# Optimization experiments

Measured on AMD Instinct MI355X. Metric: run time of the kernel, lower is better.

Reference implementation:

```python
import jax, jax.numpy as jnp
import numpy as np

B, L, H, E = 2, 2048, 16, 64  # S == L (causal self-attention), D == E


def setup_inputs() -> dict:
    key = jax.random.key(0)
    kq, kk, kv, ks = jax.random.split(key, 4)
    queries = jax.random.normal(kq, (B, L, H, E), dtype=jnp.float32)
    keys = jax.random.normal(kk, (B, L, H, E), dtype=jnp.float32)
    values = jax.random.normal(kv, (B, L, H, E), dtype=jnp.float32)
    # TriangularCausalMask: True above the diagonal -> masked out
    attn_mask = jnp.broadcast_to(
        jnp.triu(jnp.ones((L, L), dtype=bool), k=1)[None, None], (B, 1, L, L)
    )
    init_score = jax.random.uniform(ks, (B, L, L), dtype=jnp.float32)
    return {
        "queries": queries,
        "keys": keys,
        "values": values,
        "attn_mask": attn_mask,
        "init_score": init_score,
    }


def reference(queries, keys, values, attn_mask, init_score):
    # queries: [B,L,H,E], keys: [B,S,H,E], values: [B,S,H,D]
    E_ = queries.shape[-1]
    scale = 1.0 / np.sqrt(E_).astype(np.float32)
    # scores: [B,H,L,S]
    scores = jnp.einsum('blhe,bshe->bhls', queries, keys)
    scores = jnp.where(attn_mask, -jnp.inf, scores)
    A = jax.nn.softmax(scale * scores, axis=-1)  # dropout p=0 -> identity
    # post-softmax bias, broadcast over heads
    A = A + 0.1 * init_score[:, None, :, :]
    # V: [B,L,H,D]
    V = jnp.einsum('bhls,bshd->blhd', A, values)
    return V
```

## Files before the change

kernel.cpp:

```cpp
#include <hip/hip_runtime.h>
#include <hip/hip_bf16.h>
#include <math.h>

#define BB 2
#define LL 2048
#define HH 16
#define EE 64
#define LOG2E 1.44269504089f

typedef __attribute__((ext_vector_type(8))) short short8;
typedef __attribute__((ext_vector_type(4))) float floatx4;
typedef unsigned int u32;

union S8 { short8 v; u32 u[4]; ushort4 q[2]; };

__device__ inline u32 pkbf(float lo, float hi) {
    union { __hip_bfloat162 h; u32 u; } c;
    c.h = __float22bfloat162_rn(make_float2(lo, hi));
    return c.u;
}

__device__ inline ushort4 cvt4(float4 v) {
    union { __hip_bfloat162 h; u32 u; } a, b;
    a.h = __float22bfloat162_rn(make_float2(v.x, v.y));
    b.h = __float22bfloat162_rn(make_float2(v.z, v.w));
    ushort4 r;
    r.x = (unsigned short)(a.u & 0xffffu);
    r.y = (unsigned short)(a.u >> 16);
    r.z = (unsigned short)(b.u & 0xffffu);
    r.w = (unsigned short)(b.u >> 16);
    return r;
}

__device__ inline short8 pack8(float4 a, float4 b) {
    S8 s; s.q[0] = cvt4(a); s.q[1] = cvt4(b); return s.v;
}

__device__ inline void async16(unsigned short* lds, const unsigned short* g) {
    __builtin_amdgcn_global_load_lds(
        (const __attribute__((address_space(1))) u32*)g,
        (__attribute__((address_space(3))) u32*)lds, 16, 0, 0);
}

__global__ __launch_bounds__(256) void prepass(
    const float* __restrict__ k, const float* __restrict__ v,
    const float* __restrict__ isc, unsigned short* __restrict__ kb,
    unsigned short* __restrict__ vt, unsigned short* __restrict__ isb)
{
    const int bid = blockIdx.x;
    const int t = threadIdx.x;
    if (bid < 1024) {
        #pragma unroll
        for (int it = 0; it < 4; ++it) {
            int idx = bid * 1024 + it * 256 + t;
            float4 val = ((const float4*)k)[idx];
            int e4 = idx & 15, h = (idx >> 4) & 15, l = (idx >> 8) & 2047, b = idx >> 19;
            *(ushort4*)&kb[(((b * 16 + h) * 2048 + l) * 64) + e4 * 4] = cvt4(val);
        }
    } else if (bid < 2048) {
        const int ib = bid - 1024;
        #pragma unroll
        for (int it = 0; it < 8; ++it) {
            int idx = ib * 2048 + it * 256 + t;
            float4 val = ((const float4*)isc)[idx];
            val.x *= 0.1f; val.y *= 0.1f; val.z *= 0.1f; val.w *= 0.1f;
            ((ushort4*)isb)[idx] = cvt4(val);
        }
    } else {
        __shared__ float Tf[64][68];
        const int vb = bid - 2048;
        const int st = vb & 31, h = (vb >> 5) & 15, b = vb >> 9;
        const int s0 = st * 64;
        #pragma unroll
        for (int i = 0; i < 4; ++i) {
            int r = i * 16 + (t >> 4), c = (t & 15) * 4;
            float4 val = *(const float4*)(v + (((b * LL + s0 + r) * HH + h) * EE) + c);
            *(float4*)&Tf[r][c] = val;
        }
        __syncthreads();
        #pragma unroll
        for (int i = 0; i < 4; ++i) {
            int d = i * 16 + (t >> 4), s4 = (t & 15) * 4;
            float4 val = make_float4(Tf[s4 + 0][d], Tf[s4 + 1][d],
                                     Tf[s4 + 2][d], Tf[s4 + 3][d]);
            *(ushort4*)&vt[((b * 16 + h) * 64 + d) * 2048 + s0 + s4] = cvt4(val);
        }
    }
}

template <int MODE>
__device__ __forceinline__ void tile_step(
    const unsigned short* __restrict__ Ks, const unsigned short* __restrict__ Vs,
    const unsigned short* __restrict__ Is,
    const short8 qf[2], floatx4 o_attn[4], floatx4 o_bias[4], float& lsum,
    int s0, int mbase, int wave, int lq, int ln, int lnl,
    int alo, int ahi, bool hisel)
{
    u32 pk[4][2];
    if (MODE < 2) {
        #pragma unroll
        for (int sb = 0; sb < 4; ++sb) {
            if (MODE == 1 && wave < sb) { pk[sb][0] = 0; pk[sb][1] = 0; continue; }
            short8 kf0 = *(const short8*)&Ks[(sb * 16 + ln) * 64 + ((lq ^ lnl) << 3)];
            short8 kf1 = *(const short8*)&Ks[(sb * 16 + ln) * 64 + (((4 + lq) ^ lnl) << 3)];
            floatx4 sa = {0.f, 0.f, 0.f, 0.f};
            sa = __builtin_amdgcn_mfma_f32_16x16x32_bf16(kf0, qf[0], sa, 0, 0, 0);
            sa = __builtin_amdgcn_mfma_f32_16x16x32_bf16(kf1, qf[1], sa, 0, 0, 0);
            float pv[4];
            #pragma unroll
            for (int r = 0; r < 4; ++r) {
                float t = sa[r];
                if (MODE == 1 && (s0 + sb * 16 + lq * 4 + r) > (mbase + ln)) t = -INFINITY;
                float p = exp2f(t);
                lsum += p;
                pv[r] = p;
            }
            pk[sb][0] = pkbf(pv[0], pv[1]);
            pk[sb][1] = pkbf(pv[2], pv[3]);
        }
    }
    #pragma unroll
    for (int kk = 0; kk < 2; ++kk) {
        short8 vf[4];
        #pragma unroll
        for (int db = 0; db < 4; ++db)
            vf[db] = *(const short8*)&Vs[(db * 16 + ln) * 64 + (((kk * 4 + lq) ^ lnl) << 3)];
        short8 af = *(const short8*)&Is[(wave * 16 + ln) * 64 + (((kk * 4 + lq) ^ lnl) << 3)];
        #pragma unroll
        for (int db = 0; db < 4; ++db)
            o_bias[db] = __builtin_amdgcn_mfma_f32_16x16x32_bf16(af, vf[db], o_bias[db], 0, 0, 0);
        if (MODE < 2) {
            S8 pf;
            u32 a0 = (u32)__builtin_amdgcn_ds_bpermute(alo, (int)pk[kk * 2][0]);
            u32 b0 = (u32)__builtin_amdgcn_ds_bpermute(alo, (int)pk[kk * 2 + 1][0]);
            pf.u[0] = hisel ? b0 : a0;
            u32 a1 = (u32)__builtin_amdgcn_ds_bpermute(alo, (int)pk[kk * 2][1]);
            u32 b1 = (u32)__builtin_amdgcn_ds_bpermute(alo, (int)pk[kk * 2 + 1][1]);
            pf.u[1] = hisel ? b1 : a1;
            u32 a2 = (u32)__builtin_amdgcn_ds_bpermute(ahi, (int)pk[kk * 2][0]);
            u32 b2 = (u32)__builtin_amdgcn_ds_bpermute(ahi, (int)pk[kk * 2 + 1][0]);
            pf.u[2] = hisel ? b2 : a2;
            u32 a3 = (u32)__builtin_amdgcn_ds_bpermute(ahi, (int)pk[kk * 2][1]);
            u32 b3 = (u32)__builtin_amdgcn_ds_bpermute(ahi, (int)pk[kk * 2 + 1][1]);
            pf.u[3] = hisel ? b3 : a3;
            #pragma unroll
            for (int db = 0; db < 4; ++db)
                o_attn[db] = __builtin_amdgcn_mfma_f32_16x16x32_bf16(pf.v, vf[db], o_attn[db], 0, 0, 0);
        }
    }
}

__global__ __launch_bounds__(256, 3) void fused6(
    const float* __restrict__ q, const unsigned short* __restrict__ kb,
    const unsigned short* __restrict__ vt, const unsigned short* __restrict__ isb,
    float* __restrict__ out)
{
    __shared__ unsigned short Ks[2][64 * 64];
    __shared__ unsigned short Vs[2][64 * 64];
    __shared__ unsigned short Is[2][64 * 64];

    const int tid = threadIdx.x, lane = tid & 63, wave = tid >> 6;
    const int lq = lane >> 4, ln = lane & 15, lnl = ln & 7;

    const int bid = blockIdx.x;
    const int h = bid & 15, b = (bid >> 4) & 1, g = bid >> 5;
    int qt;
    if (g < 8) qt = 31 - g;
    else if (g < 16) qt = g;
    else if (g < 24) qt = 39 - g;
    else qt = g - 24;
    const int q0 = qt * 64;
    const int mbase = q0 + wave * 16;

    short8 qf[2];
    {
        const float sc = 0.125f * LOG2E;
        const float* qrow = q + (((long)(b * LL + mbase + ln)) * HH + h) * EE;
        #pragma unroll
        for (int kk = 0; kk < 2; ++kk) {
            float4 a = *(const float4*)(qrow + kk * 32 + lq * 8);
            float4 c = *(const float4*)(qrow + kk * 32 + lq * 8 + 4);
            a.x *= sc; a.y *= sc; a.z *= sc; a.w *= sc;
            c.x *= sc; c.y *= sc; c.z *= sc; c.w *= sc;
            qf[kk] = pack8(a, c);
        }
    }

    const unsigned short* kbh = kb + (long)(b * HH + h) * (LL * EE);
    const unsigned short* vth = vt + (long)(b * HH + h) * (EE * LL);

    floatx4 o_attn[4], o_bias[4];
    #pragma unroll
    for (int db = 0; db < 4; ++db) {
        o_attn[db] = (floatx4){0.f, 0.f, 0.f, 0.f};
        o_bias[db] = (floatx4){0.f, 0.f, 0.f, 0.f};
    }
    float lsum = 0.f;

    const int rr = lane >> 3, jl = lane & 7;
    const int swz = (jl ^ rr) * 8;
    const unsigned short* ksrc0 = kbh + (wave * 16 + rr) * 64 + swz;
    const unsigned short* ksrc1 = kbh + (wave * 16 + 8 + rr) * 64 + swz;
    const unsigned short* vsrc0 = vth + (wave * 16 + rr) * LL + swz;
    const unsigned short* vsrc1 = vth + (wave * 16 + 8 + rr) * LL + swz;
    const unsigned short* isrc0 = isb + (long)(b * LL + q0 + wave * 16 + rr) * LL + swz;
    const unsigned short* isrc1 = isrc0 + 8 * LL;

    const int alo = (((lq & 1) * 2) * 16 + ln) * 4;
    const int ahi = (((lq & 1) * 2 + 1) * 16 + ln) * 4;
    const bool hisel = (lq >= 2);

    auto issue = [&](int j) {
        const int s0 = j * 64, bsel = j & 1;
        if (j <= qt) {
            async16(&Ks[bsel][(wave * 16) * 64], ksrc0 + s0 * 64);
            async16(&Ks[bsel][(wave * 16 + 8) * 64], ksrc1 + s0 * 64);
        }
        async16(&Vs[bsel][(wave * 16) * 64], vsrc0 + s0);
        async16(&Vs[bsel][(wave * 16 + 8) * 64], vsrc1 + s0);
        async16(&Is[bsel][(wave * 16) * 64], isrc0 + s0);
        async16(&Is[bsel][(wave * 16 + 8) * 64], isrc1 + s0);
    };

    issue(0);
    for (int j = 0; j < qt; ++j) {
        __syncthreads();
        issue(j + 1);
        tile_step<0>(Ks[j & 1], Vs[j & 1], Is[j & 1], qf, o_attn, o_bias, lsum,
                     j * 64, mbase, wave, lq, ln, lnl, alo, ahi, hisel);
    }
    {
        __syncthreads();
        if (qt < 31) issue(qt + 1);
        tile_step<1>(Ks[qt & 1], Vs[qt & 1], Is[qt & 1], qf, o_attn, o_bias, lsum,
                     q0, mbase, wave, lq, ln, lnl, alo, ahi, hisel);
    }
    for (int j = qt + 1; j < 32; ++j) {
        __syncthreads();
        if (j < 31) issue(j + 1);
        tile_step<2>(Vs[j & 1], Vs[j & 1], Is[j & 1], qf, o_attn, o_bias, lsum,
                     j * 64, mbase, wave, lq, ln, lnl, alo, ahi, hisel);
    }

    float s = lsum;
    s += __shfl_xor(s, 16);
    s += __shfl_xor(s, 32);
    #pragma unroll
    for (int r = 0; r < 4; ++r) {
        float inv = 1.0f / __shfl(s, lq * 4 + r);
        int m = mbase + lq * 4 + r;
        float* ob = out + (((long)(b * LL + m)) * HH + h) * EE;
        #pragma unroll
        for (int db = 0; db < 4; ++db)
            ob[db * 16 + ln] = o_attn[db][r] * inv + o_bias[db][r];
    }
}

extern "C" void kernel_launch(void* const* d_in, const int* in_sizes, int n_in,
                              void* d_out, int out_size, void* d_ws, size_t ws_size,
                              hipStream_t stream) {
    (void)in_sizes; (void)n_in; (void)out_size; (void)ws_size;
    const float* q   = (const float*)d_in[0];
    const float* k   = (const float*)d_in[1];
    const float* v   = (const float*)d_in[2];
    const float* isc = (const float*)d_in[4];
    float* out = (float*)d_out;

    unsigned short* kb  = (unsigned short*)d_ws;
    unsigned short* vt  = (unsigned short*)((char*)d_ws + (8u << 20));
    unsigned short* isb = (unsigned short*)((char*)d_ws + (16u << 20));

    prepass<<<dim3(3072), dim3(256), 0, stream>>>(k, v, isc, kb, vt, isb);
    fused6<<<dim3(1024), dim3(256), 0, stream>>>(q, kb, vt, isb, out);
}
```

Before: 209.2 us.

## Load bias tile directly to registers, drop its LDS buffer, raise occupancy

The bf16 init_score bias fragments are now loaded from global memory straight into registers, one tile ahead, instead of being staged asynchronously through a double-buffered LDS tile. This removes a third of the shared-memory footprint and the LDS reads for the bias operand, which allows the launch bound to rise from 3 to 4 blocks per CU. The prepass is also widened to convert 8 floats per thread with 16-byte stores. In exchange, the per-lane global loads of the bias are less coalesced than the LDS path and add register pressure. The global load latency must also hide behind one tile of compute.

```diff
diff --git a/kernel.cpp b/kernel.cpp
--- a/kernel.cpp
+++ b/kernel.cpp
@@ -51,20 +51,23 @@
     const int t = threadIdx.x;
     if (bid < 1024) {
         #pragma unroll
-        for (int it = 0; it < 4; ++it) {
-            int idx = bid * 1024 + it * 256 + t;
-            float4 val = ((const float4*)k)[idx];
-            int e4 = idx & 15, h = (idx >> 4) & 15, l = (idx >> 8) & 2047, b = idx >> 19;
-            *(ushort4*)&kb[(((b * 16 + h) * 2048 + l) * 64) + e4 * 4] = cvt4(val);
+        for (int it = 0; it < 2; ++it) {
+            int idx = bid * 512 + it * 256 + t;
+            const float4* src = (const float4*)k + idx * 2;
+            float4 a = src[0], c = src[1];
+            int e8 = idx & 7, h = (idx >> 3) & 15, l = (idx >> 7) & 2047, b = idx >> 18;
+            *(short8*)&kb[(((b * 16 + h) * 2048 + l) * 64) + e8 * 8] = pack8(a, c);
         }
     } else if (bid < 2048) {
         const int ib = bid - 1024;
         #pragma unroll
-        for (int it = 0; it < 8; ++it) {
-            int idx = ib * 2048 + it * 256 + t;
-            float4 val = ((const float4*)isc)[idx];
-            val.x *= 0.1f; val.y *= 0.1f; val.z *= 0.1f; val.w *= 0.1f;
-            ((ushort4*)isb)[idx] = cvt4(val);
+        for (int it = 0; it < 4; ++it) {
+            int idx = ib * 1024 + it * 256 + t;
+            const float4* src = (const float4*)isc + idx * 2;
+            float4 a = src[0], c = src[1];
+            a.x *= 0.1f; a.y *= 0.1f; a.z *= 0.1f; a.w *= 0.1f;
+            c.x *= 0.1f; c.y *= 0.1f; c.z *= 0.1f; c.w *= 0.1f;
+            ((short8*)isb)[idx] = pack8(a, c);
         }
     } else {
         __shared__ float Tf[64][68];
@@ -91,8 +94,8 @@
 template <int MODE>
 __device__ __forceinline__ void tile_step(
     const unsigned short* __restrict__ Ks, const unsigned short* __restrict__ Vs,
-    const unsigned short* __restrict__ Is,
-    const short8 qf[2], floatx4 o_attn[4], floatx4 o_bias[4], float& lsum,
+    const short8 qf[2], const short8 isf[2],
+    floatx4 o_attn[4], floatx4 o_bias[4], float& lsum,
     int s0, int mbase, int wave, int lq, int ln, int lnl,
     int alo, int ahi, bool hisel)
 {
@@ -125,7 +128,7 @@
         #pragma unroll
         for (int db = 0; db < 4; ++db)
             vf[db] = *(const short8*)&Vs[(db * 16 + ln) * 64 + (((kk * 4 + lq) ^ lnl) << 3)];
-        short8 af = *(const short8*)&Is[(wave * 16 + ln) * 64 + (((kk * 4 + lq) ^ lnl) << 3)];
+        short8 af = isf[kk];
         #pragma unroll
         for (int db = 0; db < 4; ++db)
             o_bias[db] = __builtin_amdgcn_mfma_f32_16x16x32_bf16(af, vf[db], o_bias[db], 0, 0, 0);
@@ -150,14 +153,13 @@
     }
 }
 
-__global__ __launch_bounds__(256, 3) void fused6(
+__global__ __launch_bounds__(256, 4) void fused6(
     const float* __restrict__ q, const unsigned short* __restrict__ kb,
     const unsigned short* __restrict__ vt, const unsigned short* __restrict__ isb,
     float* __restrict__ out)
 {
     __shared__ unsigned short Ks[2][64 * 64];
     __shared__ unsigned short Vs[2][64 * 64];
-    __shared__ unsigned short Is[2][64 * 64];
 
     const int tid = threadIdx.x, lane = tid & 63, wave = tid >> 6;
     const int lq = lane >> 4, ln = lane & 15, lnl = ln & 7;
@@ -203,8 +205,9 @@
     const unsigned short* ksrc1 = kbh + (wave * 16 + 8 + rr) * 64 + swz;
     const unsigned short* vsrc0 = vth + (wave * 16 + rr) * LL + swz;
     const unsigned short* vsrc1 = vth + (wave * 16 + 8 + rr) * LL + swz;
-    const unsigned short* isrc0 = isb + (long)(b * LL + q0 + wave * 16 + rr) * LL + swz;
-    const unsigned short* isrc1 = isrc0 + 8 * LL;
+
+    const unsigned short* isrow =
+        isb + (long)(b * LL + q0 + wave * 16 + ln) * LL + lq * 8;
 
     const int alo = (((lq & 1) * 2) * 16 + ln) * 4;
     const int ahi = (((lq & 1) * 2 + 1) * 16 + ln) * 4;
@@ -218,28 +221,40 @@
         }
         async16(&Vs[bsel][(wave * 16) * 64], vsrc0 + s0);
         async16(&Vs[bsel][(wave * 16 + 8) * 64], vsrc1 + s0);
-        async16(&Is[bsel][(wave * 16) * 64], isrc0 + s0);
-        async16(&Is[bsel][(wave * 16 + 8) * 64], isrc1 + s0);
     };
 
+    short8 isf[2], isfn[2];
+    auto ldnext = [&](int j, short8* dst) {
+        int jc = j < 32 ? j : 31;
+        dst[0] = *(const short8*)(isrow + jc * 64);
+        dst[1] = *(const short8*)(isrow + jc * 64 + 32);
+    };
+
+    ldnext(0, isf);
     issue(0);
     for (int j = 0; j < qt; ++j) {
         __syncthreads();
         issue(j + 1);
-        tile_step<0>(Ks[j & 1], Vs[j & 1], Is[j & 1], qf, o_attn, o_bias, lsum,
+        ldnext(j + 1, isfn);
+        tile_step<0>(Ks[j & 1], Vs[j & 1], qf, isf, o_attn, o_bias, lsum,
                      j * 64, mbase, wave, lq, ln, lnl, alo, ahi, hisel);
+        isf[0] = isfn[0]; isf[1] = isfn[1];
     }
     {
         __syncthreads();
         if (qt < 31) issue(qt + 1);
-        tile_step<1>(Ks[qt & 1], Vs[qt & 1], Is[qt & 1], qf, o_attn, o_bias, lsum,
+        ldnext(qt + 1, isfn);
+        tile_step<1>(Ks[qt & 1], Vs[qt & 1], qf, isf, o_attn, o_bias, lsum,
                      q0, mbase, wave, lq, ln, lnl, alo, ahi, hisel);
+        isf[0] = isfn[0]; isf[1] = isfn[1];
     }
     for (int j = qt + 1; j < 32; ++j) {
         __syncthreads();
         if (j < 31) issue(j + 1);
-        tile_step<2>(Vs[j & 1], Vs[j & 1], Is[j & 1], qf, o_attn, o_bias, lsum,
+        ldnext(j + 1, isfn);
+        tile_step<2>(Vs[j & 1], Vs[j & 1], qf, isf, o_attn, o_bias, lsum,
                      j * 64, mbase, wave, lq, ln, lnl, alo, ahi, hisel);
+        isf[0] = isfn[0]; isf[1] = isfn[1];
     }
 
     float s = lsum;
```

Measured after the change: 197.9 us. -5.4%, faster.
